# Kernel optimization log

Hardware: AMD Instinct MI355X
Metric: run time of the kernel (lower is better)

Reference implementation:

```python
import jax
import jax.numpy as jnp
import numpy as np

N = 16384        # total input points (single batch: o = [N])
C_IN = 64        # in_planes
C_OUT = 128      # out_planes
NSAMPLE = 16     # neighbors per sampled point
STRIDE = 4       # -> new_stride = 2, FPS samples N//2 points
BN_EPS = 1e-5


def setup_inputs() -> dict:
    key = jax.random.key(0)
    k1, k2, k3 = jax.random.split(key, 3)
    p = jax.random.normal(k1, (N, 3), dtype=jnp.float32)
    x = jax.random.normal(k2, (N, C_IN), dtype=jnp.float32)
    o = jnp.array([N], dtype=jnp.int32)  # single-batch offset
    W = jax.random.normal(k3, (3 + C_IN, C_OUT), dtype=jnp.float32) * 0.05
    gamma = jnp.ones((C_OUT,), dtype=jnp.float32)
    beta = jnp.zeros((C_OUT,), dtype=jnp.float32)
    return {"p": p, "x": x, "o": o, "W": W, "gamma": gamma, "beta": beta}


def fps(p, m):
    """Furthest point sampling: returns m indices into p [N,3], starting at 0."""
    n = p.shape[0]
    def step(carry, _):
        dists, last = carry  # dists: [N] min sq-dist to selected set
        d = jnp.sum((p - p[last]) ** 2, axis=-1)
        dists = jnp.minimum(dists, d)
        nxt = jnp.argmax(dists).astype(jnp.int32)
        return (dists, nxt), nxt
    init = (jnp.full((n,), 1e10, dtype=p.dtype), jnp.int32(0))
    _, rest = jax.lax.scan(step, init, None, length=m - 1)
    return jnp.concatenate([jnp.zeros((1,), jnp.int32), rest])


def knn_idx(q, p, k):
    """Indices of k nearest points in p [N,3] for each query in q [m,3]."""
    d = (jnp.sum(q * q, -1, keepdims=True)
         - 2.0 * (q @ p.T)
         + jnp.sum(p * p, -1))  # [m, N]
    _, idx = jax.lax.top_k(-d, k)
    return idx


def group_mlp_pool(q, p, x, W, gamma, beta):
    """queryandgroup(use_xyz=True) -> linear -> BN(train) -> ReLU -> maxpool(nsample)."""
    idx = knn_idx(q, p, NSAMPLE)                      # [m, k]
    rel = p[idx] - q[:, None, :]                       # [m, k, 3] relative xyz
    feats = jnp.concatenate([rel, x[idx]], axis=-1)    # [m, k, 3+C_IN]
    h = feats @ W                                      # [m, k, C_OUT]
    # BatchNorm1d in training mode: stats over (m, k) per channel
    mean = jnp.mean(h, axis=(0, 1))
    var = jnp.var(h, axis=(0, 1))
    h = (h - mean) * jax.lax.rsqrt(var + BN_EPS) * gamma + beta
    h = jax.nn.relu(h)
    return jnp.max(h, axis=1)                          # [m, C_OUT]


def reference(p, x, o, W, gamma, beta):
    m_total = N // (STRIDE // 2)       # 8192 sampled points
    idx = fps(p, m_total)
    m1 = m_total // 2 + m_total % 2    # first half (ceil)
    idx1, idx2 = idx[:m1], idx[m1:]
    n_p, n_p2 = p[idx1], p[idx2]
    x1 = group_mlp_pool(n_p, p, x, W, gamma, beta)
    x2 = group_mlp_pool(n_p2, p, x, W, gamma, beta)
    n_o = jnp.array([m1], dtype=jnp.int32)
    n_o2 = jnp.array([m_total - m1], dtype=jnp.int32)
    return (n_p, x1, n_o, n_p2, x2, n_o2)
```

## Files before the change

### kernel.cpp

```cpp
#include <hip/hip_runtime.h>

#define N_PTS 16384
#define M_TOTAL 8192
#define M1 4096

#define OUT_NP   0
#define OUT_X1   12288
#define OUT_NO   536576
#define OUT_NP2  536577
#define OUT_X2   548865
#define OUT_NO2  1073153

#define POOL_C 64

__global__ void k0_init(const float* __restrict__ p, float* __restrict__ sump,
                        float* __restrict__ px, float* __restrict__ py, float* __restrict__ pz,
                        float* __restrict__ out, int* __restrict__ flag, int* __restrict__ fidx) {
    int i = blockIdx.x * 256 + threadIdx.x;
    if (i == 0) { out[OUT_NO] = 4096.0f; out[OUT_NO2] = 4096.0f; atomicExch(flag, 0); }
    if (i < M_TOTAL) fidx[i] = (i == 0) ? 0 : -1;
    if (i < N_PTS) {
        float x = p[3*i], y = p[3*i+1], z = p[3*i+2];
        px[i] = x; py[i] = y; pz[i] = z;
        sump[i] = __fadd_rn(__fadd_rn(__fmul_rn(x,x), __fmul_rn(y,y)), __fmul_rn(z,z));
    }
}

__device__ __forceinline__ unsigned spread4(unsigned v) {
    return (v & 1u) | ((v & 2u) << 2) | ((v & 4u) << 4) | ((v & 8u) << 6);
}
__device__ __forceinline__ float bb_d2(float qx, float qy, float qz,
                                       float mnx, float mxx, float mny, float mxy,
                                       float mnz, float mxz) {
    float ax = fmaxf(fmaxf(__fsub_rn(mnx, qx), __fsub_rn(qx, mxx)), 0.0f);
    float ay = fmaxf(fmaxf(__fsub_rn(mny, qy), __fsub_rn(qy, mxy)), 0.0f);
    float az = fmaxf(fmaxf(__fsub_rn(mnz, qz), __fsub_rn(qz, mxz)), 0.0f);
    return __fadd_rn(__fadd_rn(__fmul_rn(ax,ax), __fmul_rn(ay,ay)), __fmul_rn(az,az));
}
__device__ __forceinline__ float pt_d2(float ax, float ay, float az,
                                       float bx, float by, float bz) {
    float dx = __fsub_rn(ax,bx), dy = __fsub_rn(ay,by), dz = __fsub_rn(az,bz);
    return __fadd_rn(__fadd_rn(__fmul_rn(dx,dx), __fmul_rn(dy,dy)), __fmul_rn(dz,dz));
}
__device__ __forceinline__ float wave_max64(float v) {
    v = fmaxf(v, __int_as_float(__builtin_amdgcn_update_dpp(0, __float_as_int(v), 0x111, 0xf, 0xf, true)));
    v = fmaxf(v, __int_as_float(__builtin_amdgcn_update_dpp(0, __float_as_int(v), 0x112, 0xf, 0xf, true)));
    v = fmaxf(v, __int_as_float(__builtin_amdgcn_update_dpp(0, __float_as_int(v), 0x114, 0xf, 0xf, true)));
    v = fmaxf(v, __int_as_float(__builtin_amdgcn_update_dpp(0, __float_as_int(v), 0x118, 0xf, 0xf, true)));
    v = fmaxf(v, __int_as_float(__builtin_amdgcn_update_dpp(0, __float_as_int(v), 0x142, 0xf, 0xf, true)));
    v = fmaxf(v, __int_as_float(__builtin_amdgcn_update_dpp(0, __float_as_int(v), 0x143, 0xf, 0xf, true)));
    return __int_as_float(__builtin_amdgcn_readlane(__float_as_int(v), 63));
}

__global__ __launch_bounds__(1024) void k1_fps(
    const float* __restrict__ p,
    float* __restrict__ rx, float* __restrict__ ry, float* __restrict__ rz,
    int* __restrict__ rid,
    int* __restrict__ fidx, float* __restrict__ out, int* __restrict__ flag,
    const float* __restrict__ px, const float* __restrict__ py,
    const float* __restrict__ pz, const float* __restrict__ sump,
    int* __restrict__ knn)
{
    int tid = threadIdx.x, lane = tid & 63, wv = tid >> 6;

    __shared__ int hist[4096];
    __shared__ float sred[16][6];
    __shared__ int wsum[16];
    __shared__ float4 pool4[POOL_C];
    __shared__ unsigned ppk[POOL_C];
    __shared__ float4 barr4[POOL_C+1];
    __shared__ unsigned skeys[POOL_C];
    __shared__ float fdv[16];
    __shared__ unsigned fdk[16];
    __shared__ unsigned mcell;
    __shared__ float s_invm;
    __shared__ int s_cutbin;
    __shared__ unsigned s_cutbits;
    __shared__ unsigned s_fkey;
    __shared__ int bcnt, tcell;
    __shared__ float sdk[4][16][64];
    __shared__ int   sik[4][16][64];

    if (blockIdx.x != 0) {
        float a0 = 1.0f + tid, a1 = 2.0f, a2 = 3.0f, a3 = 4.0f;
        const float hb = 1.0000001f, hc = 1e-9f;
        if (wv < 4) {
            int g = (blockIdx.x - 1) * 4 + wv;
            for (int jq = 0; jq < 9; ++jq) {
                int q = g + 1020 * jq;
                if (q >= M_TOTAL) break;
                int qi = -1;
                for (;;) {
                    if (lane == 0)
                        qi = __hip_atomic_load(&fidx[q], __ATOMIC_RELAXED, __HIP_MEMORY_SCOPE_AGENT);
                    qi = __shfl(qi, 0);
                    if (qi >= 0) break;
#pragma unroll
                    for (int u = 0; u < 256; ++u) {
                        a0 = __fmaf_rn(a0, hb, hc); a1 = __fmaf_rn(a1, hb, hc);
                        a2 = __fmaf_rn(a2, hb, hc); a3 = __fmaf_rn(a3, hb, hc);
                    }
                }
                float qx = px[qi], qy = py[qi], qz = pz[qi], sq = sump[qi];
                float bd[16]; int bi[16];
#pragma unroll
                for (int k = 0; k < 16; ++k) { bd[k] = 3.4e38f; bi[k] = 0x7fffffff; }
                for (int j0 = 0; j0 < N_PTS; j0 += 64) {
                    int j = j0 + lane;
                    float dot = __fmaf_rn(pz[j], qz, __fmaf_rn(py[j], qy, __fmul_rn(px[j], qx)));
                    float d = __fadd_rn(__fsub_rn(sq, __fmul_rn(2.0f, dot)), sump[j]);
                    if (d < bd[15]) {
                        float cdv = d; int ci = j;
#pragma unroll
                        for (int k = 0; k < 16; ++k) {
                            if (cdv < bd[k]) { float td = bd[k]; int ti = bi[k]; bd[k] = cdv; bi[k] = ci; cdv = td; ci = ti; }
                        }
                    }
                }
#pragma unroll
                for (int k = 0; k < 16; ++k) { sdk[wv][k][lane] = bd[k]; sik[wv][k][lane] = bi[k]; }
                int pos = 0;
                for (int r = 0; r < 16; ++r) {
                    float hd = (pos < 16) ? sdk[wv][pos][lane] : 3.4e38f;
                    int   hi2 = (pos < 16) ? sik[wv][pos][lane] : 0x7fffffff;
                    float md = hd; int mi = hi2;
#pragma unroll
                    for (int off = 1; off < 64; off <<= 1) {
                        float od = __shfl_xor(md, off);
                        int   oi = __shfl_xor(mi, off);
                        if (od < md || (od == md && oi < mi)) { md = od; mi = oi; }
                    }
                    if (hi2 == mi && pos < 16) pos++;
                    if (lane == 0) knn[q*16 + r] = mi;
                }
            }
        }
        for (;;) {
#pragma unroll
            for (int u = 0; u < 512; ++u) {
                a0 = __fmaf_rn(a0, hb, hc); a1 = __fmaf_rn(a1, hb, hc);
                a2 = __fmaf_rn(a2, hb, hc); a3 = __fmaf_rn(a3, hb, hc);
            }
            int done = 0;
            if (lane == 0)
                done = __hip_atomic_load(flag, __ATOMIC_RELAXED, __HIP_MEMORY_SCOPE_AGENT);
            done = __shfl(done, 0);
            if (done) break;
        }
        __asm__ volatile("" :: "v"(a0), "v"(a1), "v"(a2), "v"(a3));
        return;
    }

    float mnx = 3.4e38f, mny = 3.4e38f, mnz = 3.4e38f;
    float mxx = -3.4e38f, mxy = -3.4e38f, mxz = -3.4e38f;
#pragma unroll
    for (int k = 0; k < 16; ++k) {
        int i = tid + 1024*k;
        float x = p[3*i], y = p[3*i+1], z = p[3*i+2];
        mnx = fminf(mnx, x); mxx = fmaxf(mxx, x);
        mny = fminf(mny, y); mxy = fmaxf(mxy, y);
        mnz = fminf(mnz, z); mxz = fmaxf(mxz, z);
    }
#pragma unroll
    for (int off = 1; off < 64; off <<= 1) {
        mnx = fminf(mnx, __shfl_xor(mnx, off)); mxx = fmaxf(mxx, __shfl_xor(mxx, off));
        mny = fminf(mny, __shfl_xor(mny, off)); mxy = fmaxf(mxy, __shfl_xor(mxy, off));
        mnz = fminf(mnz, __shfl_xor(mnz, off)); mxz = fmaxf(mxz, __shfl_xor(mxz, off));
    }
    if (lane == 0) {
        sred[wv][0] = mnx; sred[wv][1] = mxx; sred[wv][2] = mny;
        sred[wv][3] = mxy; sred[wv][4] = mnz; sred[wv][5] = mxz;
    }
    for (int j = tid; j < 4096; j += 1024) hist[j] = 0;
    __syncthreads();
    mnx = sred[0][0]; mxx = sred[0][1]; mny = sred[0][2];
    mxy = sred[0][3]; mnz = sred[0][4]; mxz = sred[0][5];
    for (int w2 = 1; w2 < 16; ++w2) {
        mnx = fminf(mnx, sred[w2][0]); mxx = fmaxf(mxx, sred[w2][1]);
        mny = fminf(mny, sred[w2][2]); mxy = fmaxf(mxy, sred[w2][3]);
        mnz = fminf(mnz, sred[w2][4]); mxz = fmaxf(mxz, sred[w2][5]);
    }
    float sx = 16.0f / fmaxf(mxx - mnx, 1e-20f);
    float sy = 16.0f / fmaxf(mxy - mny, 1e-20f);
    float sz = 16.0f / fmaxf(mxz - mnz, 1e-20f);

    int mcode[16];
#pragma unroll
    for (int k = 0; k < 16; ++k) {
        int i = tid + 1024*k;
        float x = p[3*i], y = p[3*i+1], z = p[3*i+2];
        int cx = min(15, (int)((x - mnx) * sx));
        int cy = min(15, (int)((y - mny) * sy));
        int cz = min(15, (int)((z - mnz) * sz));
        int m = (int)(spread4((unsigned)cx) | (spread4((unsigned)cy) << 1) | (spread4((unsigned)cz) << 2));
        mcode[k] = m;
        atomicAdd(&hist[m], 1);
    }
    __syncthreads();
    {
        int c0 = hist[4*tid], c1 = hist[4*tid+1], c2 = hist[4*tid+2], c3 = hist[4*tid+3];
        int lsum = c0 + c1 + c2 + c3;
        int incl = lsum;
#pragma unroll
        for (int off = 1; off < 64; off <<= 1) {
            int n = __shfl_up(incl, off);
            if (lane >= off) incl += n;
        }
        if (lane == 63) wsum[wv] = incl;
        __syncthreads();
        int woff = 0;
        for (int j = 0; j < wv; ++j) woff += wsum[j];
        int excl = woff + incl - lsum;
        hist[4*tid]   = excl;
        hist[4*tid+1] = excl + c0;
        hist[4*tid+2] = excl + c0 + c1;
        hist[4*tid+3] = excl + c0 + c1 + c2;
    }
    __syncthreads();
#pragma unroll
    for (int k = 0; k < 16; ++k) {
        int i = tid + 1024*k;
        int pos = atomicAdd(&hist[mcode[k]], 1);
        rx[pos] = p[3*i]; ry[pos] = p[3*i+1]; rz[pos] = p[3*i+2];
        rid[pos] = i;
    }
    __syncthreads();

    int base = tid * 16;
    float ld[16];
    float bmnx = 3.4e38f, bmny = 3.4e38f, bmnz = 3.4e38f;
    float bmxx = -3.4e38f, bmxy = -3.4e38f, bmxz = -3.4e38f;
#pragma unroll
    for (int k = 0; k < 16; ++k) {
        float x = rx[base+k], y = ry[base+k], z = rz[base+k];
        ld[k] = 1e10f;
        bmnx = fminf(bmnx, x); bmxx = fmaxf(bmxx, x);
        bmny = fminf(bmny, y); bmxy = fmaxf(bmxy, y);
        bmnz = fminf(bmnz, z); bmxz = fmaxf(bmxz, z);
    }
    float wsmnx = bmnx, wsmxx = bmxx, wsmny = bmny, wsmxy = bmxy, wsmnz = bmnz, wsmxz = bmxz;
#pragma unroll
    for (int off = 1; off < 64; off <<= 1) {
        wsmnx = fminf(wsmnx, __shfl_xor(wsmnx, off)); wsmxx = fmaxf(wsmxx, __shfl_xor(wsmxx, off));
        wsmny = fminf(wsmny, __shfl_xor(wsmny, off)); wsmxy = fmaxf(wsmxy, __shfl_xor(wsmxy, off));
        wsmnz = fminf(wsmnz, __shfl_xor(wsmnz, off)); wsmxz = fmaxf(wsmxz, __shfl_xor(wsmxz, off));
    }
    float gmax = 1e10f, wave_gmax = 1e10f;

    if (tid == 0) {
        float x0 = p[0], y0 = p[1], z0 = p[2];
        out[OUT_NP+0] = x0; out[OUT_NP+1] = y0; out[OUT_NP+2] = z0;
        barr4[0] = make_float4(x0, y0, z0, 0.0f);
        skeys[0] = 0u;
        bcnt = 1; tcell = 1; mcell = 0u;
    }

    for (;;) {
        __syncthreads();
        int t_now = tcell;
        int s = bcnt;
        if (tid < s)
            __hip_atomic_store(&fidx[t_now - s + tid], (int)skeys[tid], __ATOMIC_RELAXED, __HIP_MEMORY_SCOPE_AGENT);
        if (t_now >= M_TOTAL) break;

        {
            bool dirtyw = false;
            if (lane < s) {
                float4 cc = barr4[lane];
                dirtyw = bb_d2(cc.x, cc.y, cc.z, wsmnx, wsmxx, wsmny, wsmxy, wsmnz, wsmxz) < wave_gmax;
            }
            unsigned long long mm = __ballot(dirtyw);
            if (mm) {
                float gx[16], gy[16], gz[16];
#pragma unroll
                for (int k = 0; k < 16; ++k) { gx[k] = rx[base+k]; gy[k] = ry[base+k]; gz[k] = rz[base+k]; }
                while (mm) {
                    int b = __builtin_ctzll(mm); mm &= mm - 1;
                    float4 cc = barr4[b];
                    if (bb_d2(cc.x, cc.y, cc.z, bmnx, bmxx, bmny, bmxy, bmnz, bmxz) < gmax) {
#pragma unroll
                        for (int k = 0; k < 16; ++k)
                            ld[k] = fminf(ld[k], pt_d2(gx[k], gy[k], gz[k], cc.x, cc.y, cc.z));
                    }
                }
            }
        }
        gmax = ld[0];
#pragma unroll
        for (int k = 1; k < 16; ++k) gmax = fmaxf(gmax, ld[k]);
        wave_gmax = wave_max64(gmax);
        if (lane == 0) atomicMax(&mcell, __float_as_uint(wave_gmax));
        if (tid < 130) hist[tid] = 0;
        __syncthreads();
        if (tid == 0) { s_invm = 1.0f / __uint_as_float(mcell); mcell = 0u; }
        __syncthreads();
        float invm = s_invm;
#pragma unroll
        for (int k = 0; k < 16; ++k) {
            unsigned u = __float_as_uint(__fmul_rn(ld[k], invm));
            if (u >= 0x3F000000u) {
                int bin = 16256 - (int)(u >> 16);
                bin = bin < 0 ? 0 : (bin > 128 ? 128 : bin);
                atomicAdd(&hist[bin], 1);
            }
        }
        __syncthreads();
        if (wv == 0) {
            int b0 = hist[2*lane], b1 = hist[2*lane+1];
            int pair = b0 + b1;
            int incl = pair;
#pragma unroll
            for (int off = 1; off < 64; off <<= 1) { int n = __shfl_up(incl, off); if (lane >= off) incl += n; }
            int before = incl - pair;
            int cb = 0;
            if (before + b0 <= POOL_C) cb = 2*lane + 1;
            if (before + pair <= POOL_C) cb = 2*lane + 2;
            if (lane == 63) { if (incl + hist[128] <= POOL_C) cb = 129; }
#pragma unroll
            for (int off = 1; off < 64; off <<= 1) cb = max(cb, __shfl_xor(cb, off));
            if (lane == 0) { s_cutbin = cb; s_cutbits = (unsigned)(16257 - cb) << 16; }
        }
        __syncthreads();

        if (s_cutbin == 0) {
            float bv = -1.0f; unsigned bk = 0xffffffffu;
#pragma unroll
            for (int k = 0; k < 16; ++k) {
                unsigned kk = ((unsigned)rid[base+k] << 14) | (unsigned)(base + k);
                bool better = (ld[k] > bv) || (ld[k] == bv && kk < bk);
                bv = better ? ld[k] : bv; bk = better ? kk : bk;
            }
#pragma unroll
            for (int off = 1; off < 64; off <<= 1) {
                float ov = __shfl_xor(bv, off); unsigned ok = __shfl_xor(bk, off);
                bool better = (ov > bv) || (ov == bv && ok < bk);
                bv = better ? ov : bv; bk = better ? ok : bk;
            }
            if (lane == 0) { fdv[wv] = bv; fdk[wv] = bk; }
            __syncthreads();
            if (tid < 64) {
                float v2 = (tid < 16) ? fdv[tid] : -1.0f;
                unsigned k2v = (tid < 16) ? fdk[tid] : 0xffffffffu;
#pragma unroll
                for (int off = 1; off < 16; off <<= 1) {
                    float ov = __shfl_xor(v2, off); unsigned ok = __shfl_xor(k2v, off);
                    bool better = (ov > v2) || (ov == v2 && ok < k2v);
                    v2 = better ? ov : v2; k2v = better ? ok : k2v;
                }
                if (tid == 0) {
                    s_fkey = k2v;
                    int pos = (int)(k2v & 16383u);
                    __hip_atomic_store(&fidx[t_now], (int)(k2v >> 14), __ATOMIC_RELAXED, __HIP_MEMORY_SCOPE_AGENT);
                    float wx = rx[pos], wy = ry[pos], wz = rz[pos];
                    int o = (t_now < M1) ? (OUT_NP + 3*t_now) : (OUT_NP2 + 3*(t_now - M1));
                    out[o] = wx; out[o+1] = wy; out[o+2] = wz;
                    tcell = t_now + 1; bcnt = 0;
                }
            }
            __syncthreads();
            {
                int pos = (int)(s_fkey & 16383u);
                float wx = rx[pos], wy = ry[pos], wz = rz[pos];
                if (bb_d2(wx, wy, wz, bmnx, bmxx, bmny, bmxy, bmnz, bmxz) < gmax) {
#pragma unroll
                    for (int k = 0; k < 16; ++k)
                        ld[k] = fminf(ld[k], pt_d2(rx[base+k], ry[base+k], rz[base+k], wx, wy, wz));
                }
            }
            continue;
        }

        unsigned cutbits = s_cutbits;
        int cl = 0;
#pragma unroll
        for (int k = 0; k < 16; ++k)
            cl += (__float_as_uint(__fmul_rn(ld[k], invm)) >= cutbits) ? 1 : 0;
        int inc3 = cl;
#pragma unroll
        for (int off = 1; off < 64; off <<= 1) { int n = __shfl_up(inc3, off); if (lane >= off) inc3 += n; }
        if (lane == 63) wsum[wv] = inc3;
        __syncthreads();
        int woff2 = 0, ptot = 0;
        for (int j = 0; j < 16; ++j) { int wsj = wsum[j]; if (j < wv) woff2 += wsj; ptot += wsj; }
        int nb = woff2 + inc3 - cl;
#pragma unroll
        for (int k = 0; k < 16; ++k) {
            if (__float_as_uint(__fmul_rn(ld[k], invm)) >= cutbits) {
                pool4[nb] = make_float4(rx[base+k], ry[base+k], rz[base+k], ld[k]);
                ppk[nb] = (unsigned)rid[base+k];
                nb++;
            }
        }
        if (tid >= ptot && tid < POOL_C) {
            pool4[tid] = make_float4(0.0f, 0.0f, 0.0f, 0.0f);
            ppk[tid] = 0x7fffffffu;
        }
        __syncthreads();

        if (wv == 0) {
            __builtin_amdgcn_s_setprio(3);
            float4 e = pool4[lane];
            float ex = e.x, ey = e.y, ez = e.z, dv = e.w;
            unsigned key = ppk[lane];
            int tl = t_now, bc = 0;
            float mw = wave_max64(dv);
            while (__float_as_uint(__fmul_rn(mw, invm)) >= cutbits) {
                unsigned long long tie = __ballot(dv == mw);
                int wl;
                if (__popcll(tie) == 1) {
                    wl = (int)__builtin_ctzll(tie);
                } else {
                    unsigned kk = (dv == mw) ? key : 0xffffffffu;
#pragma unroll
                    for (int off = 1; off < 64; off <<= 1) kk = min(kk, (unsigned)__shfl_xor((int)kk, off));
                    tie = __ballot(dv == mw && key == kk);
                    wl = (int)__builtin_ctzll(tie);
                }
                float wx = __int_as_float(__builtin_amdgcn_readlane(__float_as_int(ex), wl));
                float wy = __int_as_float(__builtin_amdgcn_readlane(__float_as_int(ey), wl));
                float wz = __int_as_float(__builtin_amdgcn_readlane(__float_as_int(ez), wl));
                unsigned wk = (unsigned)__builtin_amdgcn_readlane((int)key, wl);
                if (lane == 0) {
                    skeys[bc] = wk;
                    int o = (tl < M1) ? (OUT_NP + 3*tl) : (OUT_NP2 + 3*(tl - M1));
                    out[o] = wx; out[o+1] = wy; out[o+2] = wz;
                    barr4[bc] = make_float4(wx, wy, wz, 0.0f);
                }
                ++bc; ++tl;
                if (tl >= M_TOTAL) break;
                dv = fminf(dv, pt_d2(ex, ey, ez, wx, wy, wz));
                mw = wave_max64(dv);
            }
            __builtin_amdgcn_s_setprio(0);
            if (lane == 0) { bcnt = bc; tcell = tl; }
        }
    }

    if (tid == 0) atomicExch(flag, 1);
}

__global__ __launch_bounds__(128) void k3_gemm(const float* __restrict__ p3, const float* __restrict__ xin,
                                               const float* __restrict__ W,
                                               const int* __restrict__ fidx, const int* __restrict__ knn,
                                               float* __restrict__ hmax, float* __restrict__ hmin,
                                               double* __restrict__ psum, double* __restrict__ psq) {
    __shared__ __align__(16) float feats[16][68];
    int c = threadIdx.x;
    int qbase = blockIdx.x * 16;
    float w[68];
#pragma unroll
    for (int j = 0; j < 67; ++j) w[j] = W[j*128 + c];
    w[67] = 0.0f;

    double s = 0.0, ss = 0.0;
    for (int qq = 0; qq < 16; ++qq) {
        int q = qbase + qq;
        int qi = fidx[q];
        float qx = p3[3*qi], qy = p3[3*qi+1], qz = p3[3*qi+2];
        for (int i = c; i < 16*68; i += 128) {
            int sIdx = i / 68, j = i - sIdx*68;
            int nj = knn[q*16 + sIdx];
            float v;
            if (j < 3) {
                float pc = p3[3*nj + j];
                float qc = (j == 0) ? qx : ((j == 1) ? qy : qz);
                v = pc - qc;
            } else if (j < 67) {
                v = xin[nj*64 + (j-3)];
            } else v = 0.0f;
            feats[sIdx][j] = v;
        }
        __syncthreads();
        float hmx = -3.4e38f, hmn = 3.4e38f;
        for (int sIdx = 0; sIdx < 16; ++sIdx) {
            float acc = 0.0f;
#pragma unroll
            for (int mm = 0; mm < 17; ++mm) {
                float4 f = *(const float4*)&feats[sIdx][4*mm];
                acc = __fmaf_rn(f.x, w[4*mm+0], acc);
                acc = __fmaf_rn(f.y, w[4*mm+1], acc);
                acc = __fmaf_rn(f.z, w[4*mm+2], acc);
                acc = __fmaf_rn(f.w, w[4*mm+3], acc);
            }
            hmx = fmaxf(hmx, acc); hmn = fminf(hmn, acc);
            s += (double)acc; ss += (double)acc * (double)acc;
        }
        hmax[q*128 + c] = hmx; hmin[q*128 + c] = hmn;
        __syncthreads();
    }
    psum[blockIdx.x*128 + c] = s;
    psq [blockIdx.x*128 + c] = ss;
}

__global__ void k35_stats(const double* __restrict__ psum, const double* __restrict__ psq,
                          const float* __restrict__ gamma, const float* __restrict__ beta,
                          float* __restrict__ scale, float* __restrict__ shift) {
    int t = threadIdx.x;
    int half = t >> 7, c = t & 127;
    double s = 0.0, ss = 0.0;
    for (int b = 0; b < 256; ++b) {
        int ib = (half*256 + b)*128 + c;
        s += psum[ib]; ss += psq[ib];
    }
    double mean = s / 65536.0;
    double var  = ss / 65536.0 - mean*mean;
    double sc   = (double)gamma[c] / sqrt(var + 1e-5);
    scale[t] = (float)sc;
    shift[t] = (float)((double)beta[c] - mean*sc);
}

__global__ __launch_bounds__(256) void k4_out(const float* __restrict__ hmax, const float* __restrict__ hmin,
                                              const float* __restrict__ scale, const float* __restrict__ shift,
                                              float* __restrict__ out) {
    int e = blockIdx.x * 256 + threadIdx.x;
    int q = e >> 7, c = e & 127;
    int half = (q >= M1) ? 1 : 0;
    float a = scale[half*128 + c], b = shift[half*128 + c];
    float v = (a >= 0.0f) ? hmax[e] : hmin[e];
    float r = fmaxf(0.0f, a*v + b);
    int off = half ? (OUT_X2 + (q - M1)*128 + c) : (OUT_X1 + q*128 + c);
    out[off] = r;
}

extern "C" void kernel_launch(void* const* d_in, const int* in_sizes, int n_in,
                              void* d_out, int out_size, void* d_ws, size_t ws_size,
                              hipStream_t stream) {
    const float* p     = (const float*)d_in[0];
    const float* x     = (const float*)d_in[1];
    const float* W     = (const float*)d_in[3];
    const float* gamma = (const float*)d_in[4];
    const float* beta  = (const float*)d_in[5];
    float* out = (float*)d_out;

    float* wsf  = (float*)d_ws;
    float* sump = wsf;
    float* px   = wsf + 16384;
    float* py   = wsf + 32768;
    float* pz   = wsf + 49152;
    int*   fidx = (int*)(wsf + 65536);
    int*   knn  = (int*)(wsf + 73728);
    float* hmax = wsf + 204800;
    float* hmin = wsf + 1253376;
    float* rxp  = hmax;
    float* ryp  = hmax + 16384;
    float* rzp  = hmax + 32768;
    int*   ridp = (int*)(hmax + 49152);
    int*   flag = (int*)(wsf + 270336);
    double* psum = (double*)((char*)d_ws + 9207808);
    double* psq  = psum + 65536;
    float* scale = (float*)(psq + 65536);
    float* shift = scale + 256;

    k0_init <<<64,   256, 0, stream>>>(p, sump, px, py, pz, out, flag, fidx);
    k1_fps  <<<256, 1024, 0, stream>>>(p, rxp, ryp, rzp, ridp, fidx, out, flag, px, py, pz, sump, knn);
    k3_gemm <<<512,  128, 0, stream>>>(p, x, W, fidx, knn, hmax, hmin, psum, psq);
    k35_stats<<<1,   256, 0, stream>>>(psum, psq, gamma, beta, scale, shift);
    k4_out  <<<4096, 256, 0, stream>>>(hmax, hmin, scale, shift, out);
}
```

Baseline: 5.482 ms.

## Cut block barriers in FPS iteration via double-buffered max and atomic pool compaction

Double-buffers the shared max cell by iteration parity so the inverse-max can be read right after one barrier, removing a separate thread-0 reduction step and its barrier. Every wave now computes the histogram cut bin redundantly instead of wave 0 broadcasting it through shared memory. Pool compaction uses an atomicAdd on a shared counter instead of a prefix scan plus a wsum barrier. The aim is fewer __syncthreads in the serial FPS loop. The trade-off is that pool order becomes nondeterministic, which tie-breaking by key must tolerate.

```diff
diff --git a/kernel.cpp b/kernel.cpp
--- a/kernel.cpp
+++ b/kernel.cpp
@@ -72,10 +72,8 @@
     __shared__ unsigned skeys[POOL_C];
     __shared__ float fdv[16];
     __shared__ unsigned fdk[16];
-    __shared__ unsigned mcell;
-    __shared__ float s_invm;
-    __shared__ int s_cutbin;
-    __shared__ unsigned s_cutbits;
+    __shared__ unsigned mcell[2];
+    __shared__ int pcnt;
     __shared__ unsigned s_fkey;
     __shared__ int bcnt, tcell;
     __shared__ float sdk[4][16][64];
@@ -252,8 +250,9 @@
         out[OUT_NP+0] = x0; out[OUT_NP+1] = y0; out[OUT_NP+2] = z0;
         barr4[0] = make_float4(x0, y0, z0, 0.0f);
         skeys[0] = 0u;
-        bcnt = 1; tcell = 1; mcell = 0u;
-    }
+        bcnt = 1; tcell = 1; mcell[0] = 0u; mcell[1] = 0u;
+    }
+    int parity = 0;
 
     for (;;) {
         __syncthreads();
@@ -262,6 +261,7 @@
         if (tid < s)
             __hip_atomic_store(&fidx[t_now - s + tid], (int)skeys[tid], __ATOMIC_RELAXED, __HIP_MEMORY_SCOPE_AGENT);
         if (t_now >= M_TOTAL) break;
+        int par = parity; parity ^= 1;
 
         {
             bool dirtyw = false;
@@ -289,12 +289,16 @@
 #pragma unroll
         for (int k = 1; k < 16; ++k) gmax = fmaxf(gmax, ld[k]);
         wave_gmax = wave_max64(gmax);
-        if (lane == 0) atomicMax(&mcell, __float_as_uint(wave_gmax));
+        if (lane == 0) atomicMax(&mcell[par], __float_as_uint(wave_gmax));
         if (tid < 130) hist[tid] = 0;
-        __syncthreads();
-        if (tid == 0) { s_invm = 1.0f / __uint_as_float(mcell); mcell = 0u; }
-        __syncthreads();
-        float invm = s_invm;
+        if (tid < POOL_C) {
+            pool4[tid] = make_float4(0.0f, 0.0f, 0.0f, 0.0f);
+            ppk[tid] = 0x7fffffffu;
+        }
+        if (tid == 0) { pcnt = 0; mcell[par ^ 1] = 0u; }
+        __syncthreads();
+
+        float invm = 1.0f / __uint_as_float(mcell[par]);
 #pragma unroll
         for (int k = 0; k < 16; ++k) {
             unsigned u = __float_as_uint(__fmul_rn(ld[k], invm));
@@ -305,24 +309,42 @@
             }
         }
         __syncthreads();
-        if (wv == 0) {
+
+        int cb;
+        {
             int b0 = hist[2*lane], b1 = hist[2*lane+1];
             int pair = b0 + b1;
             int incl = pair;
 #pragma unroll
             for (int off = 1; off < 64; off <<= 1) { int n = __shfl_up(incl, off); if (lane >= off) incl += n; }
             int before = incl - pair;
-            int cb = 0;
+            cb = 0;
             if (before + b0 <= POOL_C) cb = 2*lane + 1;
             if (before + pair <= POOL_C) cb = 2*lane + 2;
             if (lane == 63) { if (incl + hist[128] <= POOL_C) cb = 129; }
 #pragma unroll
             for (int off = 1; off < 64; off <<= 1) cb = max(cb, __shfl_xor(cb, off));
-            if (lane == 0) { s_cutbin = cb; s_cutbits = (unsigned)(16257 - cb) << 16; }
-        }
-        __syncthreads();
-
-        if (s_cutbin == 0) {
+        }
+        unsigned cutbits = (unsigned)(16257 - cb) << 16;
+        int cl = 0;
+#pragma unroll
+        for (int k = 0; k < 16; ++k)
+            cl += (__float_as_uint(__fmul_rn(ld[k], invm)) >= cutbits) ? 1 : 0;
+        if (cb != 0 && cl > 0) {
+            int nb = atomicAdd(&pcnt, cl);
+#pragma unroll
+            for (int k = 0; k < 16; ++k) {
+                if (__float_as_uint(__fmul_rn(ld[k], invm)) >= cutbits) {
+                    pool4[nb] = make_float4(rx[base+k], ry[base+k], rz[base+k], ld[k]);
+                    ppk[nb] = (unsigned)rid[base+k];
+                    nb++;
+                }
+            }
+        }
+        __syncthreads();
+        int ptot = pcnt;
+
+        if (cb == 0 || ptot == 0) {
             float bv = -1.0f; unsigned bk = 0xffffffffu;
 #pragma unroll
             for (int k = 0; k < 16; ++k) {
@@ -369,33 +391,6 @@
             }
             continue;
         }
-
-        unsigned cutbits = s_cutbits;
-        int cl = 0;
-#pragma unroll
-        for (int k = 0; k < 16; ++k)
-            cl += (__float_as_uint(__fmul_rn(ld[k], invm)) >= cutbits) ? 1 : 0;
-        int inc3 = cl;
-#pragma unroll
-        for (int off = 1; off < 64; off <<= 1) { int n = __shfl_up(inc3, off); if (lane >= off) inc3 += n; }
-        if (lane == 63) wsum[wv] = inc3;
-        __syncthreads();
-        int woff2 = 0, ptot = 0;
-        for (int j = 0; j < 16; ++j) { int wsj = wsum[j]; if (j < wv) woff2 += wsj; ptot += wsj; }
-        int nb = woff2 + inc3 - cl;
-#pragma unroll
-        for (int k = 0; k < 16; ++k) {
-            if (__float_as_uint(__fmul_rn(ld[k], invm)) >= cutbits) {
-                pool4[nb] = make_float4(rx[base+k], ry[base+k], rz[base+k], ld[k]);
-                ppk[nb] = (unsigned)rid[base+k];
-                nb++;
-            }
-        }
-        if (tid >= ptot && tid < POOL_C) {
-            pool4[tid] = make_float4(0.0f, 0.0f, 0.0f, 0.0f);
-            ppk[tid] = 0x7fffffffu;
-        }
-        __syncthreads();
 
         if (wv == 0) {
             __builtin_amdgcn_s_setprio(3);
```

Result: slower. 5.707 ms (+4.1%).
